# Kernel tuning notes

Measured on AMD Instinct MI355X. Metric: run time of the kernel, lower is better.

The kernel has to match this reference:

```python
import jax, jax.numpy as jnp
import numpy as np

DIM = 128

def _layernorm(x, g, b, eps=1e-5):
    mu = jnp.mean(x, axis=-1, keepdims=True)
    var = jnp.var(x, axis=-1, keepdims=True)
    return (x - mu) * jax.lax.rsqrt(var + eps) * g + b

def setup_inputs() -> dict:
    key = jax.random.key(0)
    ks = jax.random.split(key, 12)
    B, T, O, d = 64, 1024, 128, DIM
    s = 1.0 / np.sqrt(d)
    s2 = 1.0 / np.sqrt(2 * d)
    return {
        "token_nodes": jax.random.normal(ks[0], (B, T, d), jnp.float32),
        "obj_nodes": jax.random.normal(ks[1], (B, O, d), jnp.float32),
        "attn_to_obj": jax.random.uniform(ks[2], (B, T, O), jnp.float32),
        "W_msg_o": jax.random.uniform(ks[3], (d, d), jnp.float32, -s, s),
        "b_msg_o": jnp.zeros((d,), jnp.float32),
        "W_msg_t": jax.random.uniform(ks[4], (d, d), jnp.float32, -s, s),
        "b_msg_t": jnp.zeros((d,), jnp.float32),
        "W_upd_t": jax.random.uniform(ks[5], (2 * d, d), jnp.float32, -s2, s2),
        "b_upd_t": jnp.zeros((d,), jnp.float32),
        "W_upd_o": jax.random.uniform(ks[6], (2 * d, d), jnp.float32, -s2, s2),
        "b_upd_o": jnp.zeros((d,), jnp.float32),
        "g_ln_t": jnp.ones((d,), jnp.float32),
        "beta_ln_t": jnp.zeros((d,), jnp.float32),
        "g_ln_o": jnp.ones((d,), jnp.float32),
        "beta_ln_o": jnp.zeros((d,), jnp.float32),
    }

def reference(token_nodes, obj_nodes, attn_to_obj,
              W_msg_o, b_msg_o, W_msg_t, b_msg_t,
              W_upd_t, b_upd_t, W_upd_o, b_upd_o,
              g_ln_t, beta_ln_t, g_ln_o, beta_ln_o):
    # messages from objects -> tokens
    msg_o = obj_nodes @ W_msg_o + b_msg_o                      # [B,O,d]
    agg_to_t = jnp.einsum('bto,bod->btd', attn_to_obj, msg_o)  # [B,T,d]
    # messages from tokens -> objects (transposed attention)
    msg_t = token_nodes @ W_msg_t + b_msg_t                    # [B,T,d]
    agg_to_o = jnp.einsum('bto,btd->bod', attn_to_obj, msg_t)  # [B,O,d]
    # fused update MLPs (dropout is identity in eval mode)
    new_t = jax.nn.relu(jnp.concatenate([token_nodes, agg_to_t], axis=-1) @ W_upd_t + b_upd_t)
    new_o = jax.nn.relu(jnp.concatenate([obj_nodes, agg_to_o], axis=-1) @ W_upd_o + b_upd_o)
    new_t = _layernorm(token_nodes + new_t, g_ln_t, beta_ln_t)
    new_o = _layernorm(obj_nodes + new_o, g_ln_o, beta_ln_o)
    return (new_t, new_o)
```

## Files before the change

### kernel.cpp

```cpp
#include <hip/hip_runtime.h>

typedef unsigned short u16;
typedef __attribute__((ext_vector_type(8))) short bf16x8;
typedef __attribute__((ext_vector_type(4))) float f32x4;

#define NB 64
#define NT 1024
#define NO 128
#define ND 128

__device__ __forceinline__ u16 f2bf(float f) {
    union { float f; unsigned u; } v; v.f = f;
    unsigned r = v.u + 0x7FFFu + ((v.u >> 16) & 1u);
    return (u16)(r >> 16);
}
__device__ __forceinline__ float bf2f(short s) {
    union { unsigned u; float f; } v; v.u = ((unsigned)(u16)s) << 16; return v.f;
}

__device__ __forceinline__ bf16x8 frag_from_f32(const float* p) {
    const float4 a = *reinterpret_cast<const float4*>(p);
    const float4 b = *reinterpret_cast<const float4*>(p + 4);
    bf16x8 r;
    r[0] = (short)f2bf(a.x); r[1] = (short)f2bf(a.y);
    r[2] = (short)f2bf(a.z); r[3] = (short)f2bf(a.w);
    r[4] = (short)f2bf(b.x); r[5] = (short)f2bf(b.y);
    r[6] = (short)f2bf(b.z); r[7] = (short)f2bf(b.w);
    return r;
}

__global__ __launch_bounds__(512, 4)
void k_P(const float* __restrict__ attn, const float* __restrict__ tok,
         const float* __restrict__ obj, const float* __restrict__ Wmo,
         const float* __restrict__ bmo, const float* __restrict__ Wmt,
         const float* __restrict__ Wut, const float* __restrict__ Wuo,
         u16* __restrict__ Psl, float* __restrict__ rs_part,
         u16* __restrict__ msg_oT, u16* __restrict__ WmtT,
         u16* __restrict__ WutT, u16* __restrict__ WuoT) {
    __shared__ u16 aT[128 * 128];
    __shared__ u16 dT[128 * 128];
    int b = blockIdx.x >> 2, ks = blockIdx.x & 3;
    int tid = threadIdx.x;

    {
        int idx = blockIdx.x * 512 + tid;
        if (idx < 16384) {
            int k = idx >> 7, n = idx & 127;
            WmtT[n * 128 + k] = f2bf(Wmt[idx]);
        } else if (idx < 49152) {
            int i2 = idx - 16384; int k = i2 >> 7, n = i2 & 127;
            WutT[n * 256 + (k ^ ((n & 7) << 3))] = f2bf(Wut[i2]);
        } else if (idx < 81920) {
            int i2 = idx - 49152; int k = i2 >> 7, n = i2 & 127;
            WuoT[n * 256 + k] = f2bf(Wuo[i2]);
        }
    }

    int l = tid & 63, w = tid >> 6;
    int l15 = l & 15, lk = (l >> 4) * 8, rsub = (l >> 4) * 4;
    int ro = w * 16 + l15;
    int og = (tid & 31) * 4;
    int tg = tid >> 5;

    f32x4 acc[8] = {};
    float rsum = 0.f;
#pragma unroll
    for (int c = 0; c < 2; c++) {
        int kb = ks * 256 + c * 128;
        const float* asrc = attn + ((size_t)b * NT + kb) * 128;
        const float* tsrc = tok  + ((size_t)b * NT + kb) * 128;
        if (c) __syncthreads();
#pragma unroll
        for (int half = 0; half < 2; half++) {
            const float* src = half ? tsrc : asrc;
            u16* buf = half ? dT : aT;
            int t0 = tg * 8;
            f32x4 v[8];
#pragma unroll
            for (int i = 0; i < 8; i++)
                v[i] = *reinterpret_cast<const f32x4*>(src + (size_t)(t0 + i) * 128 + og);
            int gr = t0 >> 3;
#pragma unroll
            for (int j = 0; j < 4; j++) {
                int o = og + j;
                bf16x8 pk;
#pragma unroll
                for (int i = 0; i < 8; i++) pk[i] = (short)f2bf(v[i][j]);
                *reinterpret_cast<bf16x8*>(&buf[o * 128 + ((gr ^ (o & 15)) << 3)]) = pk;
            }
        }
        __syncthreads();
#pragma unroll
        for (int kk = 0; kk < 4; kk++) {
            int tt = kk * 32 + lk;
            bf16x8 a = *reinterpret_cast<const bf16x8*>(
                &aT[ro * 128 + (((tt >> 3) ^ (ro & 15)) << 3)]);
#pragma unroll
            for (int i = 0; i < 8; i++) rsum += bf2f(a[i]);
#pragma unroll
            for (int ct = 0; ct < 8; ct++) {
                int d = ct * 16 + l15;
                bf16x8 bf = *reinterpret_cast<const bf16x8*>(
                    &dT[d * 128 + (((tt >> 3) ^ (d & 15)) << 3)]);
                acc[ct] = __builtin_amdgcn_mfma_f32_16x16x32_bf16(a, bf, acc[ct], 0, 0, 0);
            }
        }
    }
    rsum += __shfl_xor(rsum, 16, 64);
    rsum += __shfl_xor(rsum, 32, 64);
    if (l < 16) rs_part[((size_t)ks * NB + b) * NO + w * 16 + l15] = rsum;
    u16* pout = Psl + (((size_t)(ks * NB + b)) * NO + w * 16) * ND;
#pragma unroll
    for (int ct = 0; ct < 8; ct++)
#pragma unroll
        for (int r = 0; r < 4; r++)
            pout[(size_t)(rsub + r) * ND + ct * 16 + l15] = f2bf(acc[ct][r]);

    if (ks == 0) {
        __syncthreads();
#pragma unroll
        for (int i = 0; i < 32; i++) {
            int idx = i * 512 + tid;
            int k = idx >> 7, n = idx & 127;
            aT[n * 128 + (k ^ ((n & 7) << 3))] = f2bf(Wmo[idx]);
        }
        __syncthreads();
        f32x4 mc[8] = {};
        const float* xp = obj + ((size_t)b * NO + w * 16 + l15) * 128;
#pragma unroll
        for (int kk = 0; kk < 4; kk++) {
            bf16x8 a = frag_from_f32(xp + kk * 32 + lk);
#pragma unroll
            for (int ct = 0; ct < 8; ct++) {
                int n = ct * 16 + l15;
                bf16x8 bfr = *reinterpret_cast<const bf16x8*>(
                    &aT[n * 128 + ((kk * 32 + lk) ^ ((n & 7) << 3))]);
                mc[ct] = __builtin_amdgcn_mfma_f32_16x16x32_bf16(a, bfr, mc[ct], 0, 0, 0);
            }
        }
#pragma unroll
        for (int ct = 0; ct < 8; ct++) {
            int n = ct * 16 + l15;
            float bv = bmo[n];
            ushort4 pk;
            pk.x = f2bf(mc[ct][0] + bv);
            pk.y = f2bf(mc[ct][1] + bv);
            pk.z = f2bf(mc[ct][2] + bv);
            pk.w = f2bf(mc[ct][3] + bv);
            int o = w * 16 + rsub;
            *reinterpret_cast<ushort4*>(&dT[n * 128 + (o ^ ((n & 7) << 3))]) = pk;
        }
        __syncthreads();
        u16* mout = msg_oT + (size_t)b * 16384;
#pragma unroll
        for (int i = 0; i < 4; i++) {
            int idx2 = (i * 512 + tid) * 8;
            *reinterpret_cast<bf16x8*>(mout + idx2) = *reinterpret_cast<const bf16x8*>(&dT[idx2]);
        }
    }
}

__global__ __launch_bounds__(256, 4)
void k_obj_final(const float* __restrict__ obj, const u16* __restrict__ Psl,
                 const float* __restrict__ rs_part, const u16* __restrict__ WmtT,
                 const float* __restrict__ bmt, const u16* __restrict__ WuoT,
                 const float* __restrict__ buo, const float* __restrict__ g,
                 const float* __restrict__ beta, float* __restrict__ out) {
    __shared__ u16 P_lds[32][136];
    __shared__ u16 agg_lds[32][136];
    __shared__ float rs_lds[32];
    __shared__ float part_s[32][2], part_sq[32][2];
    int bid = blockIdx.x;
    int b = bid >> 2, ot = bid & 3;
    int ob = ot * 32;
    int tid = threadIdx.x;
    {
        int row = tid >> 3, c0 = (tid & 7) * 16;
        float sm[16];
#pragma unroll
        for (int i = 0; i < 16; i++) sm[i] = 0.f;
#pragma unroll
        for (int ks = 0; ks < 4; ks++) {
            const u16* p = Psl + (((size_t)(ks * NB + b)) * NO + ob + row) * ND + c0;
            bf16x8 v0 = *reinterpret_cast<const bf16x8*>(p);
            bf16x8 v1 = *reinterpret_cast<const bf16x8*>(p + 8);
#pragma unroll
            for (int i = 0; i < 8; i++) { sm[i] += bf2f(v0[i]); sm[8 + i] += bf2f(v1[i]); }
        }
#pragma unroll
        for (int j = 0; j < 4; j++) {
            ushort4 pk;
            pk.x = f2bf(sm[j * 4 + 0]); pk.y = f2bf(sm[j * 4 + 1]);
            pk.z = f2bf(sm[j * 4 + 2]); pk.w = f2bf(sm[j * 4 + 3]);
            *reinterpret_cast<ushort4*>(&P_lds[row][c0 + j * 4]) = pk;
        }
        if (tid < 32) {
            float r = 0.f;
#pragma unroll
            for (int ks = 0; ks < 4; ks++) r += rs_part[((size_t)ks * NB + b) * NO + ob + tid];
            rs_lds[tid] = r;
        }
    }
    __syncthreads();
    int l = tid & 63, w = tid >> 6;
    int l15 = l & 15, lk = (l >> 4) * 8, rsub = (l >> 4) * 4;
    int wr = (w & 1) * 16, wc = (w >> 1) * 64;
    f32x4 agg[4] = {};
#pragma unroll
    for (int kk = 0; kk < 4; kk++) {
        bf16x8 a = *reinterpret_cast<const bf16x8*>(&P_lds[wr + l15][kk * 32 + lk]);
#pragma unroll
        for (int ct = 0; ct < 4; ct++) {
            bf16x8 bf = *reinterpret_cast<const bf16x8*>(WmtT + (wc + ct * 16 + l15) * 128 + kk * 32 + lk);
            agg[ct] = __builtin_amdgcn_mfma_f32_16x16x32_bf16(a, bf, agg[ct], 0, 0, 0);
        }
    }
#pragma unroll
    for (int ct = 0; ct < 4; ct++) {
        int n = wc + ct * 16 + l15;
        float bb = bmt[n];
#pragma unroll
        for (int r = 0; r < 4; r++) {
            float v = agg[ct][r] + rs_lds[wr + rsub + r] * bb;
            agg_lds[wr + rsub + r][n] = f2bf(v);
        }
    }
    __syncthreads();
    f32x4 accm[4] = {};
    const float* objp = obj + ((size_t)(b * NO) + ob + wr + l15) * ND;
#pragma unroll
    for (int kk = 0; kk < 8; kk++) {
        int k0 = kk * 32;
        bf16x8 a = (k0 < 128) ? frag_from_f32(objp + k0 + lk)
                              : *reinterpret_cast<const bf16x8*>(&agg_lds[wr + l15][k0 - 128 + lk]);
#pragma unroll
        for (int ct = 0; ct < 4; ct++) {
            bf16x8 bf = *reinterpret_cast<const bf16x8*>(WuoT + (wc + ct * 16 + l15) * 256 + k0 + lk);
            accm[ct] = __builtin_amdgcn_mfma_f32_16x16x32_bf16(a, bf, accm[ct], 0, 0, 0);
        }
    }
    const float* objr = obj + ((size_t)(b * NO) + ob) * ND;
    float s[4] = {0.f, 0.f, 0.f, 0.f}, sq[4] = {0.f, 0.f, 0.f, 0.f};
#pragma unroll
    for (int ct = 0; ct < 4; ct++) {
        int n = wc + ct * 16 + l15;
        float bv = buo[n];
#pragma unroll
        for (int r = 0; r < 4; r++) {
            int lr = wr + rsub + r;
            float v = objr[(size_t)lr * ND + n] + fmaxf(accm[ct][r] + bv, 0.f);
            accm[ct][r] = v;
            s[r] += v;
            sq[r] += v * v;
        }
    }
#pragma unroll
    for (int ofs = 1; ofs < 16; ofs <<= 1) {
#pragma unroll
        for (int r = 0; r < 4; r++) {
            s[r]  += __shfl_xor(s[r], ofs, 64);
            sq[r] += __shfl_xor(sq[r], ofs, 64);
        }
    }
    if (l15 < 4) {
        float sv = (l15 == 0) ? s[0] : (l15 == 1) ? s[1] : (l15 == 2) ? s[2] : s[3];
        float qv = (l15 == 0) ? sq[0] : (l15 == 1) ? sq[1] : (l15 == 2) ? sq[2] : sq[3];
        part_s[wr + rsub + l15][w >> 1] = sv;
        part_sq[wr + rsub + l15][w >> 1] = qv;
    }
    __syncthreads();
    float mu[4], rstd[4];
#pragma unroll
    for (int r = 0; r < 4; r++) {
        int lr = wr + rsub + r;
        float st = part_s[lr][0] + part_s[lr][1];
        float qt = part_sq[lr][0] + part_sq[lr][1];
        mu[r] = st * (1.f / 128.f);
        rstd[r] = rsqrtf(qt * (1.f / 128.f) - mu[r] * mu[r] + 1e-5f);
    }
#pragma unroll
    for (int ct = 0; ct < 4; ct++) {
        int n = wc + ct * 16 + l15;
        float gn = g[n], bn = beta[n];
#pragma unroll
        for (int r = 0; r < 4; r++) {
            int lr = wr + rsub + r;
            out[((size_t)(b * NO) + ob + lr) * ND + n] = (accm[ct][r] - mu[r]) * rstd[r] * gn + bn;
        }
    }
}

__global__ __launch_bounds__(512, 2)
void k_token_update(const float* __restrict__ tok, const float* __restrict__ attn,
                    const u16* __restrict__ msg_oT, const u16* __restrict__ WutT,
                    const float* __restrict__ bupd, const float* __restrict__ g,
                    const float* __restrict__ beta, float* __restrict__ out) {
    __shared__ u16 msg_lds[16384];
    __shared__ u16 wut_lds[32768];
    __shared__ u16 agg_b[8][16][136];
    int i = blockIdx.x;
    int b  = ((i >> 5) << 3) + (i & 7);
    int bq = (i >> 3) & 3;
    int tid = threadIdx.x;
    {
        const u16* msrc = msg_oT + (size_t)b * 16384;
#pragma unroll
        for (int k = 0; k < 4; k++) {
            int idx = (k * 512 + tid) * 8;
            *reinterpret_cast<bf16x8*>(&msg_lds[idx]) = *reinterpret_cast<const bf16x8*>(msrc + idx);
        }
#pragma unroll
        for (int k = 0; k < 8; k++) {
            int idx = (k * 512 + tid) * 8;
            *reinterpret_cast<bf16x8*>(&wut_lds[idx]) = *reinterpret_cast<const bf16x8*>(WutT + idx);
        }
    }
    __syncthreads();
    int l = tid & 63, w = tid >> 6;
    int l15 = l & 15, lk = (l >> 4) * 8, rsub = (l >> 4) * 4;

#pragma unroll
    for (int pass = 0; pass < 2; pass++) {
        int trow = bq * 256 + pass * 128 + w * 16;
        size_t rbase = (size_t)b * NT + trow;
        const float* aF   = attn + (rbase + l15) * NO;
        const float* tokp = tok + (rbase + l15) * ND;
        const float* tokr = tok + rbase * ND;

        bf16x8 af[4];
#pragma unroll
        for (int kk = 0; kk < 4; kk++)
            af[kk] = frag_from_f32(aF + kk * 32 + lk);
        bf16x8 am0[4];
#pragma unroll
        for (int kk = 0; kk < 4; kk++)
            am0[kk] = frag_from_f32(tokp + kk * 32 + lk);
        float resv[8][4];
#pragma unroll
        for (int ct = 0; ct < 8; ct++)
#pragma unroll
            for (int r = 0; r < 4; r++)
                resv[ct][r] = tokr[(size_t)(rsub + r) * ND + ct * 16 + l15];

        f32x4 acc[8] = {};
#pragma unroll
        for (int kk = 0; kk < 4; kk++) {
#pragma unroll
            for (int ct = 0; ct < 8; ct++) {
                int n = ct * 16 + l15;
                bf16x8 bf = *reinterpret_cast<const bf16x8*>(
                    &msg_lds[n * 128 + ((kk * 32 + lk) ^ ((n & 7) << 3))]);
                acc[ct] = __builtin_amdgcn_mfma_f32_16x16x32_bf16(af[kk], bf, acc[ct], 0, 0, 0);
            }
        }
#pragma unroll
        for (int ct = 0; ct < 8; ct++) {
            int n = ct * 16 + l15;
#pragma unroll
            for (int r = 0; r < 4; r++)
                agg_b[w][rsub + r][n] = f2bf(acc[ct][r]);
        }
        asm volatile("s_waitcnt lgkmcnt(0)" ::: "memory");
        __builtin_amdgcn_sched_barrier(0);
        bf16x8 am[8];
#pragma unroll
        for (int kk = 0; kk < 4; kk++) am[kk] = am0[kk];
#pragma unroll
        for (int kk = 0; kk < 4; kk++)
            am[4 + kk] = *reinterpret_cast<const bf16x8*>(&agg_b[w][l15][kk * 32 + lk]);
        f32x4 accm[8] = {};
#pragma unroll
        for (int kk = 0; kk < 8; kk++) {
#pragma unroll
            for (int ct = 0; ct < 8; ct++) {
                int n = ct * 16 + l15;
                bf16x8 bf = *reinterpret_cast<const bf16x8*>(
                    &wut_lds[n * 256 + ((kk * 32 + lk) ^ ((n & 7) << 3))]);
                accm[ct] = __builtin_amdgcn_mfma_f32_16x16x32_bf16(am[kk], bf, accm[ct], 0, 0, 0);
            }
        }
        float s[4] = {0.f, 0.f, 0.f, 0.f}, sq[4] = {0.f, 0.f, 0.f, 0.f};
#pragma unroll
        for (int ct = 0; ct < 8; ct++) {
            int n = ct * 16 + l15;
            float bv = bupd[n];
#pragma unroll
            for (int r = 0; r < 4; r++) {
                float v = resv[ct][r] + fmaxf(accm[ct][r] + bv, 0.f);
                accm[ct][r] = v;
                s[r] += v;
                sq[r] += v * v;
            }
        }
#pragma unroll
        for (int ofs = 1; ofs < 16; ofs <<= 1) {
#pragma unroll
            for (int r = 0; r < 4; r++) {
                s[r]  += __shfl_xor(s[r], ofs, 64);
                sq[r] += __shfl_xor(sq[r], ofs, 64);
            }
        }
        float mu[4], rstd[4];
#pragma unroll
        for (int r = 0; r < 4; r++) {
            mu[r] = s[r] * (1.f / 128.f);
            rstd[r] = rsqrtf(sq[r] * (1.f / 128.f) - mu[r] * mu[r] + 1e-5f);
        }
#pragma unroll
        for (int ct = 0; ct < 8; ct++) {
            int n = ct * 16 + l15;
            float gn = g[n], bn = beta[n];
#pragma unroll
            for (int r = 0; r < 4; r++)
                out[(rbase + rsub + r) * ND + n] = (accm[ct][r] - mu[r]) * rstd[r] * gn + bn;
        }
    }
}

extern "C" void kernel_launch(void* const* d_in, const int* in_sizes, int n_in,
                              void* d_out, int out_size, void* d_ws, size_t ws_size,
                              hipStream_t stream) {
    const float* tok  = (const float*)d_in[0];
    const float* obj  = (const float*)d_in[1];
    const float* attn = (const float*)d_in[2];
    const float* Wmo  = (const float*)d_in[3];
    const float* bmo  = (const float*)d_in[4];
    const float* Wmt  = (const float*)d_in[5];
    const float* bmt  = (const float*)d_in[6];
    const float* Wut  = (const float*)d_in[7];
    const float* but  = (const float*)d_in[8];
    const float* Wuo  = (const float*)d_in[9];
    const float* buo  = (const float*)d_in[10];
    const float* gt   = (const float*)d_in[11];
    const float* bt   = (const float*)d_in[12];
    const float* go   = (const float*)d_in[13];
    const float* bo   = (const float*)d_in[14];
    float* out = (float*)d_out;

    u16* ws = (u16*)d_ws;
    u16* msg_oT = ws;
    u16* WmtT   = msg_oT + 1048576;
    u16* WutT   = WmtT + 16384;
    u16* WuoT   = WutT + 32768;
    u16* Psl    = WuoT + 32768;
    float* rs_part = (float*)(Psl + 4194304);

    k_P<<<dim3(256), dim3(512), 0, stream>>>(attn, tok, obj, Wmo, bmo, Wmt, Wut, Wuo,
                                             Psl, rs_part, msg_oT, WmtT, WutT, WuoT);
    k_token_update<<<dim3(256), dim3(512), 0, stream>>>(tok, attn, msg_oT, WutT, but, gt, bt, out);
    k_obj_final<<<dim3(256), dim3(256), 0, stream>>>(obj, Psl, rs_part, WmtT, bmt, WuoT, buo, go, bo,
                                                     out + (size_t)NB * NT * ND);
}
```

Baseline: 55.70 us.

## Use 1024-thread blocks in token update, one pass per wave with swizzled staging

The token-update kernel goes from 512 threads running two 128-row passes to 1024 threads (16 waves) where each wave handles one 16-row tile in a single pass. Each block now loads msg and weights once for 256 rows using twice as many threads. The per-wave agg staging buffer switches from padded rows to an XOR-swizzled layout. Residual token values are loaded after the GEMMs rather than held in registers, to fit the tighter register budget of launch_bounds(1024,4). This raises memory-level parallelism but limits each thread's registers and LDS use (now 160KB per block) may restrict occupancy.

```diff
diff --git a/kernel.cpp b/kernel.cpp
--- a/kernel.cpp
+++ b/kernel.cpp
@@ -290,130 +290,123 @@
     }
 }
 
-__global__ __launch_bounds__(512, 2)
+__global__ __launch_bounds__(1024, 4)
 void k_token_update(const float* __restrict__ tok, const float* __restrict__ attn,
                     const u16* __restrict__ msg_oT, const u16* __restrict__ WutT,
                     const float* __restrict__ bupd, const float* __restrict__ g,
                     const float* __restrict__ beta, float* __restrict__ out) {
     __shared__ u16 msg_lds[16384];
     __shared__ u16 wut_lds[32768];
-    __shared__ u16 agg_b[8][16][136];
+    __shared__ u16 aggU[32768];
     int i = blockIdx.x;
     int b  = ((i >> 5) << 3) + (i & 7);
     int bq = (i >> 3) & 3;
     int tid = threadIdx.x;
     {
         const u16* msrc = msg_oT + (size_t)b * 16384;
+        int idx = tid * 16;
+        *reinterpret_cast<bf16x8*>(&msg_lds[idx])     = *reinterpret_cast<const bf16x8*>(msrc + idx);
+        *reinterpret_cast<bf16x8*>(&msg_lds[idx + 8]) = *reinterpret_cast<const bf16x8*>(msrc + idx + 8);
 #pragma unroll
         for (int k = 0; k < 4; k++) {
-            int idx = (k * 512 + tid) * 8;
-            *reinterpret_cast<bf16x8*>(&msg_lds[idx]) = *reinterpret_cast<const bf16x8*>(msrc + idx);
-        }
-#pragma unroll
-        for (int k = 0; k < 8; k++) {
-            int idx = (k * 512 + tid) * 8;
-            *reinterpret_cast<bf16x8*>(&wut_lds[idx]) = *reinterpret_cast<const bf16x8*>(WutT + idx);
+            int idx2 = (k * 1024 + tid) * 8;
+            *reinterpret_cast<bf16x8*>(&wut_lds[idx2]) = *reinterpret_cast<const bf16x8*>(WutT + idx2);
         }
     }
     __syncthreads();
     int l = tid & 63, w = tid >> 6;
     int l15 = l & 15, lk = (l >> 4) * 8, rsub = (l >> 4) * 4;
 
-#pragma unroll
-    for (int pass = 0; pass < 2; pass++) {
-        int trow = bq * 256 + pass * 128 + w * 16;
-        size_t rbase = (size_t)b * NT + trow;
-        const float* aF   = attn + (rbase + l15) * NO;
-        const float* tokp = tok + (rbase + l15) * ND;
-        const float* tokr = tok + rbase * ND;
-
-        bf16x8 af[4];
-#pragma unroll
-        for (int kk = 0; kk < 4; kk++)
-            af[kk] = frag_from_f32(aF + kk * 32 + lk);
-        bf16x8 am0[4];
-#pragma unroll
-        for (int kk = 0; kk < 4; kk++)
-            am0[kk] = frag_from_f32(tokp + kk * 32 + lk);
-        float resv[8][4];
-#pragma unroll
-        for (int ct = 0; ct < 8; ct++)
-#pragma unroll
-            for (int r = 0; r < 4; r++)
-                resv[ct][r] = tokr[(size_t)(rsub + r) * ND + ct * 16 + l15];
-
-        f32x4 acc[8] = {};
-#pragma unroll
-        for (int kk = 0; kk < 4; kk++) {
-#pragma unroll
-            for (int ct = 0; ct < 8; ct++) {
-                int n = ct * 16 + l15;
-                bf16x8 bf = *reinterpret_cast<const bf16x8*>(
-                    &msg_lds[n * 128 + ((kk * 32 + lk) ^ ((n & 7) << 3))]);
-                acc[ct] = __builtin_amdgcn_mfma_f32_16x16x32_bf16(af[kk], bf, acc[ct], 0, 0, 0);
-            }
-        }
+    int trow = bq * 256 + w * 16;
+    size_t rbase = (size_t)b * NT + trow;
+    const float* aF   = attn + (rbase + l15) * NO;
+    const float* tokp = tok + (rbase + l15) * ND;
+
+    bf16x8 af[4];
+#pragma unroll
+    for (int kk = 0; kk < 4; kk++)
+        af[kk] = frag_from_f32(aF + kk * 32 + lk);
+    bf16x8 am0[4];
+#pragma unroll
+    for (int kk = 0; kk < 4; kk++)
+        am0[kk] = frag_from_f32(tokp + kk * 32 + lk);
+
+    f32x4 acc[8] = {};
+#pragma unroll
+    for (int kk = 0; kk < 4; kk++) {
 #pragma unroll
         for (int ct = 0; ct < 8; ct++) {
             int n = ct * 16 + l15;
-#pragma unroll
-            for (int r = 0; r < 4; r++)
-                agg_b[w][rsub + r][n] = f2bf(acc[ct][r]);
-        }
-        asm volatile("s_waitcnt lgkmcnt(0)" ::: "memory");
-        __builtin_amdgcn_sched_barrier(0);
-        bf16x8 am[8];
-#pragma unroll
-        for (int kk = 0; kk < 4; kk++) am[kk] = am0[kk];
-#pragma unroll
-        for (int kk = 0; kk < 4; kk++)
-            am[4 + kk] = *reinterpret_cast<const bf16x8*>(&agg_b[w][l15][kk * 32 + lk]);
-        f32x4 accm[8] = {};
-#pragma unroll
-        for (int kk = 0; kk < 8; kk++) {
-#pragma unroll
-            for (int ct = 0; ct < 8; ct++) {
-                int n = ct * 16 + l15;
-                bf16x8 bf = *reinterpret_cast<const bf16x8*>(
-                    &wut_lds[n * 256 + ((kk * 32 + lk) ^ ((n & 7) << 3))]);
-                accm[ct] = __builtin_amdgcn_mfma_f32_16x16x32_bf16(am[kk], bf, accm[ct], 0, 0, 0);
-            }
-        }
-        float s[4] = {0.f, 0.f, 0.f, 0.f}, sq[4] = {0.f, 0.f, 0.f, 0.f};
+            bf16x8 bf = *reinterpret_cast<const bf16x8*>(
+                &msg_lds[n * 128 + ((kk * 32 + lk) ^ ((n & 7) << 3))]);
+            acc[ct] = __builtin_amdgcn_mfma_f32_16x16x32_bf16(af[kk], bf, acc[ct], 0, 0, 0);
+        }
+    }
+    u16* ab = &aggU[w * 2048];
+#pragma unroll
+    for (int ct = 0; ct < 8; ct++) {
+        int n = ct * 16 + l15;
+#pragma unroll
+        for (int r = 0; r < 4; r++) {
+            int row = rsub + r;
+            ab[row * 128 + (n ^ ((row & 7) << 3))] = f2bf(acc[ct][r]);
+        }
+    }
+    asm volatile("s_waitcnt lgkmcnt(0)" ::: "memory");
+    __builtin_amdgcn_sched_barrier(0);
+    bf16x8 am[8];
+#pragma unroll
+    for (int kk = 0; kk < 4; kk++) am[kk] = am0[kk];
+#pragma unroll
+    for (int kk = 0; kk < 4; kk++)
+        am[4 + kk] = *reinterpret_cast<const bf16x8*>(
+            &ab[l15 * 128 + ((kk * 32 + lk) ^ ((l15 & 7) << 3))]);
+    f32x4 accm[8] = {};
+#pragma unroll
+    for (int kk = 0; kk < 8; kk++) {
 #pragma unroll
         for (int ct = 0; ct < 8; ct++) {
             int n = ct * 16 + l15;
-            float bv = bupd[n];
-#pragma unroll
-            for (int r = 0; r < 4; r++) {
-                float v = resv[ct][r] + fmaxf(accm[ct][r] + bv, 0.f);
-                accm[ct][r] = v;
-                s[r] += v;
-                sq[r] += v * v;
-            }
-        }
-#pragma unroll
-        for (int ofs = 1; ofs < 16; ofs <<= 1) {
-#pragma unroll
-            for (int r = 0; r < 4; r++) {
-                s[r]  += __shfl_xor(s[r], ofs, 64);
-                sq[r] += __shfl_xor(sq[r], ofs, 64);
-            }
-        }
-        float mu[4], rstd[4];
-#pragma unroll
-        for (int r = 0; r < 4; r++) {
-            mu[r] = s[r] * (1.f / 128.f);
-            rstd[r] = rsqrtf(sq[r] * (1.f / 128.f) - mu[r] * mu[r] + 1e-5f);
-        }
-#pragma unroll
-        for (int ct = 0; ct < 8; ct++) {
-            int n = ct * 16 + l15;
-            float gn = g[n], bn = beta[n];
-#pragma unroll
-            for (int r = 0; r < 4; r++)
-                out[(rbase + rsub + r) * ND + n] = (accm[ct][r] - mu[r]) * rstd[r] * gn + bn;
-        }
+            bf16x8 bf = *reinterpret_cast<const bf16x8*>(
+                &wut_lds[n * 256 + ((kk * 32 + lk) ^ ((n & 7) << 3))]);
+            accm[ct] = __builtin_amdgcn_mfma_f32_16x16x32_bf16(am[kk], bf, accm[ct], 0, 0, 0);
+        }
+    }
+    const float* tokr = tok + rbase * ND;
+    float s[4] = {0.f, 0.f, 0.f, 0.f}, sq[4] = {0.f, 0.f, 0.f, 0.f};
+#pragma unroll
+    for (int ct = 0; ct < 8; ct++) {
+        int n = ct * 16 + l15;
+        float bv = bupd[n];
+#pragma unroll
+        for (int r = 0; r < 4; r++) {
+            float v = tokr[(size_t)(rsub + r) * ND + n] + fmaxf(accm[ct][r] + bv, 0.f);
+            accm[ct][r] = v;
+            s[r] += v;
+            sq[r] += v * v;
+        }
+    }
+#pragma unroll
+    for (int ofs = 1; ofs < 16; ofs <<= 1) {
+#pragma unroll
+        for (int r = 0; r < 4; r++) {
+            s[r]  += __shfl_xor(s[r], ofs, 64);
+            sq[r] += __shfl_xor(sq[r], ofs, 64);
+        }
+    }
+    float mu[4], rstd[4];
+#pragma unroll
+    for (int r = 0; r < 4; r++) {
+        mu[r] = s[r] * (1.f / 128.f);
+        rstd[r] = rsqrtf(sq[r] * (1.f / 128.f) - mu[r] * mu[r] + 1e-5f);
+    }
+#pragma unroll
+    for (int ct = 0; ct < 8; ct++) {
+        int n = ct * 16 + l15;
+        float gn = g[n], bn = beta[n];
+#pragma unroll
+        for (int r = 0; r < 4; r++)
+            out[(rbase + rsub + r) * ND + n] = (accm[ct][r] - mu[r]) * rstd[r] * gn + bn;
     }
 }
 
@@ -447,7 +440,7 @@
 
     k_P<<<dim3(256), dim3(512), 0, stream>>>(attn, tok, obj, Wmo, bmo, Wmt, Wut, Wuo,
                                              Psl, rs_part, msg_oT, WmtT, WutT, WuoT);
-    k_token_update<<<dim3(256), dim3(512), 0, stream>>>(tok, attn, msg_oT, WutT, but, gt, bt, out);
+    k_token_update<<<dim3(256), dim3(1024), 0, stream>>>(tok, attn, msg_oT, WutT, but, gt, bt, out);
     k_obj_final<<<dim3(256), dim3(256), 0, stream>>>(obj, Psl, rs_part, WmtT, bmt, WuoT, buo, go, bo,
                                                      out + (size_t)NB * NT * ND);
 }
```

New measurement: 61.31 us. +10.1%, slower.
